# Kernel tuning notes

Measured on AMD Instinct MI355X. Metric: run time of the kernel, lower is better.

## Reference

```python
import jax, jax.numpy as jnp
import numpy as np

BS, Q, NC, T = 8, 500, 2, 400


def setup_inputs() -> dict:
    key = jax.random.key(0)
    k1, k2, k3, k4, k5 = jax.random.split(key, 5)
    pred_logits = jax.random.normal(k1, (BS, Q, NC), dtype=jnp.float32)
    pred_keypoints = jax.random.normal(k2, (BS, Q, 53), dtype=jnp.float32)
    tgt_ids = jax.random.randint(k3, (T,), 0, NC)
    # target keypoints: [center(2) | offsets(34)] ~ N(0, .2), visibility(17) in {0,1}
    tgt_xy = 0.2 * jax.random.normal(k4, (T, 36), dtype=jnp.float32)
    tgt_vis = jax.random.randint(k5, (T, 17), 0, 2).astype(jnp.float32)
    tgt_keypoints = jnp.concatenate([tgt_xy, tgt_vis], axis=1)
    return {"pred_logits": pred_logits, "pred_keypoints": pred_keypoints,
            "tgt_ids": tgt_ids, "tgt_keypoints": tgt_keypoints, "num_boxes": T}


def reference(pred_logits, pred_keypoints, tgt_ids, tgt_keypoints, num_boxes):
    """Fused batched cost-matrix construction of HungarianMatcher.forward.
    Returns C of shape [bs, num_queries, total_targets] (the matrix handed to
    scipy linear_sum_assignment in the original)."""
    cost_class_w, l_deltas, l_vis, l_ctr, l_abs = 1.0, 0.5, 0.2, 0.5, 4.0
    bs, q, nc = pred_logits.shape
    nb = jnp.asarray(num_boxes, jnp.float32)

    out_prob = jax.nn.softmax(pred_logits.reshape(-1, nc), axis=-1)   # [N, NC]
    kp = pred_keypoints.reshape(-1, 53)                               # [N, 53]
    C_pred, Z_pred, V_pred = kp[:, :2], kp[:, 2:36], kp[:, 36:]
    C_gt, Z_gt, V_gt = tgt_keypoints[:, :2], tgt_keypoints[:, 2:36], tgt_keypoints[:, 36:]

    t = tgt_keypoints.shape[0]
    # absolute keypoint positions: tile center per keypoint then add offsets
    A_gt = jnp.tile(C_gt[:, None, :], (1, 17, 1)).reshape(t, 34) + Z_gt       # [T, 34]
    A_pred = jnp.tile(C_pred[:, None, :], (1, 17, 1)).reshape(-1, 34) + Z_pred  # [N, 34]

    cost_class = -out_prob[:, tgt_ids]                                # [N, T]
    Vgt_ = jnp.repeat(V_gt, 2, axis=1)                                # [T, 34]

    # visibility-masked L1 distances (fuses the per-target cdist loop)
    offset_loss = jnp.sum(jnp.abs((Z_pred[:, None, :] - Z_gt[None, :, :]) * Vgt_[None, :, :]), axis=-1) / nb
    abs_loss = jnp.sum(jnp.abs((A_pred[:, None, :] - A_gt[None, :, :]) * Vgt_[None, :, :]), axis=-1) / nb
    # squared-L2 distances
    viz_loss = jnp.sum((V_pred[:, None, :] - V_gt[None, :, :]) ** 2, axis=-1) / nb
    center_loss = jnp.sum((C_pred[:, None, :] - C_gt[None, :, :]) ** 2, axis=-1) / nb

    C = (cost_class_w * cost_class + l_deltas * offset_loss + l_vis * viz_loss
         + l_ctr * center_loss + l_abs * abs_loss)
    return C.reshape(bs, q, t)
```

## Files before the change

### kernel.cpp

```cpp
#include <hip/hip_runtime.h>

#define P_TOT 4000
#define T_TOT 400
#define PP    8
#define BD    448

__global__ __launch_bounds__(BD, 3) void hm_cost_kernel(
    const float* __restrict__ logits,
    const float* __restrict__ kp,
    const int*   __restrict__ tgt_ids,
    const float* __restrict__ tk,
    const int*   __restrict__ num_boxes,
    float*       __restrict__ out)
{
    const int t      = threadIdx.x;
    const bool valid = (t < T_TOT);
    const int tc     = valid ? t : (T_TOT - 1);

    const float nbinv = 1.0f / (float)(*num_boxes);

    const float* trow = tk + tc * 53;
    const float Cg0 = trow[0];
    const float Cg1 = trow[1];
    float Zg[34];
#pragma unroll
    for (int k = 0; k < 34; ++k) Zg[k] = trow[2 + k];
    float Vg[17];
    float sVg = 0.f;
#pragma unroll
    for (int j = 0; j < 17; ++j) {
        Vg[j] = trow[36 + j];
        sVg += Vg[j] * Vg[j];
    }
    const bool cls1 = (tgt_ids[tc] != 0);

    const int pbase = blockIdx.x * PP;

#pragma unroll 1
    for (int pi = 0; pi < PP; ++pi) {
        const int p = pbase + pi;
        const float* prow = kp + p * 53;

        const float l0 = logits[2 * p];
        const float l1 = logits[2 * p + 1];
        const float q  = __expf(l1 - l0);
        const float p0 = 1.0f / (1.0f + q);
        const float prob = cls1 ? (q * p0) : p0;

        const float dc0 = prow[0] - Cg0;
        const float dc1 = prow[1] - Cg1;

        float off = 0.f, ab = 0.f, vv = 0.f, sVp = 0.f;
#pragma unroll
        for (int j = 0; j < 17; ++j) {
            const float v   = Vg[j];
            const float zp0 = prow[2 + 2 * j];
            const float zp1 = prow[3 + 2 * j];
            const float dz0 = zp0 - Zg[2 * j];
            const float dz1 = zp1 - Zg[2 * j + 1];
            off += (fabsf(dz0) + fabsf(dz1)) * v;
            ab  += (fabsf(dz0 + dc0) + fabsf(dz1 + dc1)) * v;
            const float vp = prow[36 + j];
            vv  += vp * v;
            sVp += vp * vp;
        }

        const float viz = sVp - 2.f * vv + sVg;
        const float ctr = dc0 * dc0 + dc1 * dc1;

        const float c = -prob
                      + (0.5f * off + 4.0f * ab + 0.2f * viz + 0.5f * ctr) * nbinv;

        if (valid) out[p * T_TOT + t] = c;
    }
}

extern "C" void kernel_launch(void* const* d_in, const int* in_sizes, int n_in,
                              void* d_out, int out_size, void* d_ws, size_t ws_size,
                              hipStream_t stream) {
    const float* logits    = (const float*)d_in[0];
    const float* kp        = (const float*)d_in[1];
    const int*   tgt_ids   = (const int*)  d_in[2];
    const float* tk        = (const float*)d_in[3];
    const int*   num_boxes = (const int*)  d_in[4];
    float*       out       = (float*)d_out;

    hm_cost_kernel<<<P_TOT / PP, BD, 0, stream>>>(logits, kp, tgt_ids, tk,
                                                  num_boxes, out);
}
```

Baseline: 78.12 us.

## Tile targets across a 2D grid and stage target rows in shared memory

Splits the 400 targets into two tiles of 200 over a 2D grid and shrinks the block from 448 to 256 threads. Each block copies its target tile into LDS with float4 loads before threads read their per-target registers, which avoids strided per-thread global reads of 53-float rows. The prediction loop is unrolled by two. In exchange, 56 of 256 threads per block sit idle, there are twice as many blocks, and each block now pays for a shared-memory fill and a barrier.

Measured after the change: 88.01 us. +12.7%, slower.

```diff
diff --git a/kernel.cpp b/kernel.cpp
--- a/kernel.cpp
+++ b/kernel.cpp
@@ -1,9 +1,10 @@
 #include <hip/hip_runtime.h>
 
-#define P_TOT 4000
-#define T_TOT 400
-#define PP    8
-#define BD    448
+#define P_TOT  4000
+#define T_TOT  400
+#define T_TILE 200
+#define PP     8
+#define BD     256
 
 __global__ __launch_bounds__(BD, 3) void hm_cost_kernel(
     const float* __restrict__ logits,
@@ -13,13 +14,26 @@
     const int*   __restrict__ num_boxes,
     float*       __restrict__ out)
 {
-    const int t      = threadIdx.x;
-    const bool valid = (t < T_TOT);
-    const int tc     = valid ? t : (T_TOT - 1);
+    __shared__ float s_tk[T_TILE * 53];
+
+    {
+        const float4* __restrict__ src4 =
+            (const float4*)(tk + blockIdx.x * (T_TILE * 53));
+        float4* dst4 = (float4*)s_tk;
+#pragma unroll
+        for (int i = threadIdx.x; i < (T_TILE * 53) / 4; i += BD)
+            dst4[i] = src4[i];
+    }
+    __syncthreads();
+
+    const int tl     = threadIdx.x;
+    const bool valid = (tl < T_TILE);
+    const int tlc    = valid ? tl : (T_TILE - 1);
+    const int tg     = blockIdx.x * T_TILE + tlc;
 
     const float nbinv = 1.0f / (float)(*num_boxes);
 
-    const float* trow = tk + tc * 53;
+    const float* trow = &s_tk[tlc * 53];
     const float Cg0 = trow[0];
     const float Cg1 = trow[1];
     float Zg[34];
@@ -32,14 +46,14 @@
         Vg[j] = trow[36 + j];
         sVg += Vg[j] * Vg[j];
     }
-    const bool cls1 = (tgt_ids[tc] != 0);
+    const bool cls1 = (tgt_ids[tg] != 0);
 
-    const int pbase = blockIdx.x * PP;
+    const int pbase = blockIdx.y * PP;
 
-#pragma unroll 1
+#pragma unroll 2
     for (int pi = 0; pi < PP; ++pi) {
         const int p = pbase + pi;
-        const float* prow = kp + p * 53;
+        const float* __restrict__ prow = kp + p * 53;
 
         const float l0 = logits[2 * p];
         const float l1 = logits[2 * p + 1];
@@ -54,10 +68,8 @@
 #pragma unroll
         for (int j = 0; j < 17; ++j) {
             const float v   = Vg[j];
-            const float zp0 = prow[2 + 2 * j];
-            const float zp1 = prow[3 + 2 * j];
-            const float dz0 = zp0 - Zg[2 * j];
-            const float dz1 = zp1 - Zg[2 * j + 1];
+            const float dz0 = prow[2 + 2 * j]     - Zg[2 * j];
+            const float dz1 = prow[3 + 2 * j]     - Zg[2 * j + 1];
             off += (fabsf(dz0) + fabsf(dz1)) * v;
             ab  += (fabsf(dz0 + dc0) + fabsf(dz1 + dc1)) * v;
             const float vp = prow[36 + j];
@@ -71,7 +83,7 @@
         const float c = -prob
                       + (0.5f * off + 4.0f * ab + 0.2f * viz + 0.5f * ctr) * nbinv;
 
-        if (valid) out[p * T_TOT + t] = c;
+        if (valid) out[p * T_TOT + blockIdx.x * T_TILE + tl] = c;
     }
 }
 
@@ -85,6 +97,7 @@
     const int*   num_boxes = (const int*)  d_in[4];
     float*       out       = (float*)d_out;
 
-    hm_cost_kernel<<<P_TOT / PP, BD, 0, stream>>>(logits, kp, tgt_ids, tk,
-                                                  num_boxes, out);
+    dim3 grid(T_TOT / T_TILE, P_TOT / PP);
+    hm_cost_kernel<<<grid, BD, 0, stream>>>(logits, kp, tgt_ids, tk,
+                                            num_boxes, out);
 }
```
